# Kernel tuning notes

Measured on AMD Instinct MI355X. Metric: run time of the kernel, lower is better.

The kernel has to match this reference:

```python
import jax, jax.numpy as jnp
import numpy as np

B, N, D, H = 4, 1024, 256, 8  # batch, seq, in_dim(=per-head qkv_dim), n_heads


def setup_inputs() -> dict:
    key = jax.random.key(0)
    k1, k2, k3 = jax.random.split(key, 3)
    x = jax.random.normal(k1, (B, N, D), dtype=jnp.float32)
    Wqkv = jax.random.normal(k2, (D, 3 * D * H), dtype=jnp.float32) * 0.02
    bqkv = jnp.zeros((3 * D * H,), dtype=jnp.float32)
    W0 = jax.random.normal(k3, (D * H, D), dtype=jnp.float32) * 0.02
    b0 = jnp.zeros((D,), dtype=jnp.float32)
    return {"x": x, "Wqkv": Wqkv, "bqkv": bqkv, "W0": W0, "b0": b0}


def reference(x, Wqkv, bqkv, W0, b0):
    b, n, d = x.shape
    h = Wqkv.shape[1] // (3 * d)
    qkv = x @ Wqkv + bqkv                      # [b, n, 3*d*h]
    # Faithful to torch: raw row-major reinterpretation of the buffer.
    q, k, v = jnp.reshape(qkv, (3, b, n, d, h))
    score = jnp.einsum('bnqh,btqh->bnth', q, k) * (d ** -0.5)  # [b, n, n, h]
    attn = jax.nn.softmax(score, axis=1)       # softmax over query axis (dim=1), as in source
    # einsum 'bnnh,bnqh->bnqh' = diagonal of attn times v (faithful to source)
    av = jnp.einsum('bnnh,bnqh->bnqh', attn, v)  # [b, n, d, h]
    out = av.reshape(b, n, d * h) @ W0 + b0    # [b, n, d]
    return out
```

## Files before the change

kernel.cpp:

```cpp
#include <hip/hip_runtime.h>


#define SEGSZ 8388608

typedef short v8s __attribute__((ext_vector_type(8)));
typedef float v4f __attribute__((ext_vector_type(4)));

__device__ __forceinline__ ushort f2bf(float v) {
  union { float f; unsigned u; } x; x.f = v;
  const unsigned r = x.u + 0x7fff + ((x.u >> 16) & 1);
  return (ushort)(r >> 16);
}
__device__ __forceinline__ float bf2f(ushort v) {
  union { unsigned u; float f; } x; x.u = ((unsigned)v) << 16;
  return x.f;
}

#define GLOAD_LDS16(g, l)                                            \
  __builtin_amdgcn_global_load_lds(                                  \
      (const __attribute__((address_space(1))) void*)(g),            \
      (__attribute__((address_space(3))) void*)(l), 16, 0, 0)

__global__ __launch_bounds__(256) void prep(
    const float* __restrict__ X, const float* __restrict__ Wqkv,
    const float* __restrict__ W0, ushort* __restrict__ xb,
    ushort* __restrict__ whT, ushort* __restrict__ w0T) {
  __shared__ float T[64][65];
  const int tid = threadIdx.x;
  int bid = blockIdx.x;

  if (bid < 1024) {
    const size_t i = ((size_t)bid * 256 + tid) * 4;
    const float4 v = *(const float4*)&X[i];
    ushort4 hv = {f2bf(v.x), f2bf(v.y), f2bf(v.z), f2bf(v.w)};
    *(ushort4*)&xb[i] = hv;
    return;
  }
  bid -= 1024;
  if (bid < 384) {
    const int n0 = (bid % 96) * 64;
    const int k0 = (bid / 96) * 64;
    {
      const int row = tid >> 2;
      const int c0 = (tid & 3) * 16;
#pragma unroll
      for (int j = 0; j < 16; j += 4) {
        const float4 v = *(const float4*)&Wqkv[(size_t)(k0 + row) * 6144 + n0 + c0 + j];
        T[row][c0 + j + 0] = v.x; T[row][c0 + j + 1] = v.y;
        T[row][c0 + j + 2] = v.z; T[row][c0 + j + 3] = v.w;
      }
    }
    __syncthreads();
    {
      const int nn = tid >> 2;
      const int kk0 = (tid & 3) * 16;
      const int n = n0 + nn;
      const int seg = n >> 11, h = n & 7, d = (n & 2047) >> 3;
      const int p = seg * 2048 + h * 256 + d;
      ushort hv[16];
#pragma unroll
      for (int j = 0; j < 16; ++j) hv[j] = f2bf(T[kk0 + j][nn]);
      const size_t base = (size_t)p * 256 + k0 + kk0;
#pragma unroll
      for (int j = 0; j < 16; j += 8) *(v8s*)&whT[base + j] = *(v8s*)&hv[j];
    }
    return;
  }
  bid -= 384;
  {
    const int e0 = (bid & 3) * 64;
    const int k0 = (bid >> 2) * 64;
    {
      const int row = tid >> 2;
      const int c0 = (tid & 3) * 16;
#pragma unroll
      for (int j = 0; j < 16; j += 4) {
        const float4 v = *(const float4*)&W0[(size_t)(k0 + row) * 256 + e0 + c0 + j];
        T[row][c0 + j + 0] = v.x; T[row][c0 + j + 1] = v.y;
        T[row][c0 + j + 2] = v.z; T[row][c0 + j + 3] = v.w;
      }
    }
    __syncthreads();
    {
      const int ee = tid >> 2;
      const int kk0 = (tid & 3) * 16;
#pragma unroll
      for (int j = 0; j < 16; ++j) {
        const int k = k0 + kk0 + j;
        const int d = k >> 3, h = k & 7;
        w0T[(size_t)(e0 + ee) * 2048 + h * 256 + d] = f2bf(T[kk0 + j][ee]);
      }
    }
  }
}

__global__ __launch_bounds__(512) void qkv_mfma(
    const ushort* __restrict__ xb, const ushort* __restrict__ whT,
    const float* __restrict__ bias, ushort* __restrict__ qkvb) {
  __shared__ ushort As[256 * 32];
  __shared__ ushort Bh[128 * 32];
  const int tid = threadIdx.x;
  const int wave = tid >> 6, lane = tid & 63;
  const int quad = lane >> 4, l15 = lane & 15;
  const int c0 = blockIdx.x * 128;
  const int r0 = blockIdx.y * 256;
  const int wr = (wave >> 1) * 64;
  const int wc = (wave & 1) * 64;

  v4f acc[4][4] = {};

  for (int d0 = 0; d0 < 256; d0 += 32) {
#pragma unroll
    for (int h2 = 0; h2 < 2; ++h2) {
      const int rr = wave * 32 + h2 * 16;
      const int row = rr + (lane >> 2);
      GLOAD_LDS16(xb + (size_t)(r0 + row) * 256 + d0 + (lane & 3) * 8, &As[rr * 32]);
    }
    {
      const int rr = wave * 16;
      const int row = rr + (lane >> 2);
      GLOAD_LDS16(whT + (size_t)(c0 + row) * 256 + d0 + (lane & 3) * 8, &Bh[rr * 32]);
    }
    __syncthreads();

    v8s aF[4], bF[4];
#pragma unroll
    for (int i = 0; i < 4; ++i) {
      aF[i] = *(const v8s*)&As[(wr + i * 16 + l15) * 32 + quad * 8];
      bF[i] = *(const v8s*)&Bh[(wc + i * 16 + l15) * 32 + quad * 8];
    }
#pragma unroll
    for (int ri = 0; ri < 4; ++ri)
#pragma unroll
      for (int ci = 0; ci < 4; ++ci)
        acc[ri][ci] = __builtin_amdgcn_mfma_f32_16x16x32_bf16(
            aF[ri], bF[ci], acc[ri][ci], 0, 0, 0);
    __syncthreads();
  }

#pragma unroll
  for (int ci = 0; ci < 4; ++ci) {
    const int c = c0 + wc + ci * 16 + l15;
    const int cseg = c >> 11;
    const int h = (c & 2047) >> 8;
    const int d = c & 255;
    const float bv = bias[cseg * 2048 + d * 8 + h];
#pragma unroll
    for (int ri = 0; ri < 4; ++ri)
#pragma unroll
      for (int rg = 0; rg < 4; ++rg) {
        const int r = r0 + wr + ri * 16 + quad * 4 + rg;
        const int g = r * 3 + cseg;
        const int seg = g >> 12;
        const int tok = g & 4095;
        float val = acc[ri][ci][rg] + bv;
        if (seg == 0) val *= 0.0625f;
        qkvb[(size_t)seg * SEGSZ + (size_t)tok * 2048 + h * 256 + d] = f2bf(val);
      }
  }
}

__global__ __launch_bounds__(256) void scores_mfma(
    const ushort* __restrict__ qkvb, float* __restrict__ pl,
    float* __restrict__ sd_ws) {
  __shared__ ushort Ks[8 * 128 * 32];
  __shared__ ushort Qs[128 * 32];
  __shared__ float redL[2][2][64];

  const int tid = threadIdx.x;
  const int wave = tid >> 6, lane = tid & 63;
  const int quad = lane >> 4, l15 = lane & 15;
  const int bh = blockIdx.z * 8 + blockIdx.x;
  const int strip = blockIdx.y;
  const int tt0 = (strip >> 1) * 128;
  const int half = strip & 1;
  const int b = bh >> 3, h = bh & 7;
  const ushort* Qg = qkvb + (size_t)b * 1024 * 2048 + h * 256;
  const ushort* Kg = Qg + SEGSZ;

  const int wr = (wave >> 1) * 64;
  const int wc = (wave & 1) * 64;

#pragma unroll
  for (int c = 0; c < 8; ++c)
#pragma unroll
    for (int h2 = 0; h2 < 2; ++h2) {
      const int rr = wave * 32 + h2 * 16;
      const int row = rr + (lane >> 2);
      GLOAD_LDS16(Kg + (size_t)(tt0 + row) * 2048 + c * 32 + (lane & 3) * 8,
                  &Ks[c * 4096 + rr * 32]);
    }

  float colsum[4] = {0.f, 0.f, 0.f, 0.f};

  for (int i = 0; i < 4; ++i) {
    const int nn0 = half * 512 + i * 128;
    v4f acc[4][4] = {};
#pragma unroll
    for (int c = 0; c < 8; ++c) {
#pragma unroll
      for (int h2 = 0; h2 < 2; ++h2) {
        const int rr = wave * 32 + h2 * 16;
        const int row = rr + (lane >> 2);
        GLOAD_LDS16(Qg + (size_t)(nn0 + row) * 2048 + c * 32 + (lane & 3) * 8,
                    &Qs[rr * 32]);
      }
      __syncthreads();

      v8s aF[4], bF[4];
#pragma unroll
      for (int j = 0; j < 4; ++j) {
        aF[j] = *(const v8s*)&Qs[(wr + j * 16 + l15) * 32 + quad * 8];
        bF[j] = *(const v8s*)&Ks[c * 4096 + (wc + j * 16 + l15) * 32 + quad * 8];
      }
#pragma unroll
      for (int ri = 0; ri < 4; ++ri)
#pragma unroll
        for (int ci = 0; ci < 4; ++ci)
          acc[ri][ci] = __builtin_amdgcn_mfma_f32_16x16x32_bf16(
              aF[ri], bF[ci], acc[ri][ci], 0, 0, 0);
      __syncthreads();
    }
#pragma unroll
    for (int ci = 0; ci < 4; ++ci) {
      float s = 0.f;
#pragma unroll
      for (int ri = 0; ri < 4; ++ri)
#pragma unroll
        for (int rg = 0; rg < 4; ++rg) s += __expf(acc[ri][ci][rg]);
      colsum[ci] += s;
    }
    if (nn0 == tt0 && (wave == 0 || wave == 3) && quad == (l15 >> 2)) {
#pragma unroll
      for (int ri = 0; ri < 4; ++ri) {
        const int t = tt0 + (wave & 1) * 64 + ri * 16 + l15;
        sd_ws[(size_t)bh * 1024 + t] = acc[ri][ri][l15 & 3];
      }
    }
  }

#pragma unroll
  for (int ci = 0; ci < 4; ++ci) {
    colsum[ci] += __shfl_xor(colsum[ci], 16, 64);
    colsum[ci] += __shfl_xor(colsum[ci], 32, 64);
  }
  if (quad == 0) {
#pragma unroll
    for (int ci = 0; ci < 4; ++ci)
      redL[wave & 1][wave >> 1][ci * 16 + l15] = colsum[ci];
  }
  __syncthreads();
  if ((wave >> 1) == 0 && quad == 0) {
#pragma unroll
    for (int ci = 0; ci < 4; ++ci) {
      const int t = tt0 + (wave & 1) * 64 + ci * 16 + l15;
      const float l = colsum[ci] + redL[wave & 1][1][ci * 16 + l15];
      pl[((size_t)bh * 1024 + t) * 2 + half] = l;
    }
  }
}

template <bool ATOMIC>
__global__ __launch_bounds__(512) void av_mfma(
    const ushort* __restrict__ vb, const ushort* __restrict__ w0T,
    const float* __restrict__ pl, const float* __restrict__ sd,
    ushort* __restrict__ partial, float* __restrict__ out) {
  __shared__ ushort As[128 * 32];
  __shared__ ushort Bs[256 * 32];
  __shared__ float diagS[128];
  const int tid = threadIdx.x;
  const int wave = tid >> 6, lane = tid & 63;
  const int quad = lane >> 4, l15 = lane & 15;
  const int tok0 = blockIdx.x * 128;
  const int h = blockIdx.y;
  const int kbase = h * 256;
  const int wr = (wave >> 2) * 64;
  const int wc = (wave & 3) * 64;

  if (tid < 128) {
    const int bh = (tok0 >> 10) * 8 + h;
    const int t = (tok0 & 1023) + tid;
    const size_t base = ((size_t)bh * 1024 + t) * 2;
    diagS[tid] = __expf(sd[(size_t)bh * 1024 + t]) / (pl[base] + pl[base + 1]);
  }

  v4f acc[4][4] = {};

  for (int d0 = 0; d0 < 256; d0 += 32) {
    {
      const int rr = wave * 16;
      const int row = rr + (lane >> 2);
      GLOAD_LDS16(vb + (size_t)(tok0 + row) * 2048 + kbase + d0 + (lane & 3) * 8,
                  &As[rr * 32]);
    }
#pragma unroll
    for (int h2 = 0; h2 < 2; ++h2) {
      const int rr = wave * 32 + h2 * 16;
      const int row = rr + (lane >> 2);
      GLOAD_LDS16(w0T + (size_t)row * 2048 + kbase + d0 + (lane & 3) * 8,
                  &Bs[rr * 32]);
    }
    __syncthreads();

    v8s aF[4], bF[4];
#pragma unroll
    for (int i = 0; i < 4; ++i) {
      aF[i] = *(const v8s*)&As[(wr + i * 16 + l15) * 32 + quad * 8];
      bF[i] = *(const v8s*)&Bs[(wc + i * 16 + l15) * 32 + quad * 8];
    }
#pragma unroll
    for (int ri = 0; ri < 4; ++ri)
#pragma unroll
      for (int ci = 0; ci < 4; ++ci)
        acc[ri][ci] =
            __builtin_amdgcn_mfma_f32_16x16x32_bf16(aF[ri], bF[ci], acc[ri][ci], 0, 0, 0);
    __syncthreads();
  }

#pragma unroll
  for (int ri = 0; ri < 4; ++ri)
#pragma unroll
    for (int rg = 0; rg < 4; ++rg) {
      const int lrow = wr + ri * 16 + quad * 4 + rg;
      const int tok = tok0 + lrow;
      const float dg = diagS[lrow];
#pragma unroll
      for (int ci = 0; ci < 4; ++ci) {
        const int e = wc + ci * 16 + l15;
        const float val = acc[ri][ci][rg] * dg;
        if (ATOMIC)
          atomicAdd(&out[(size_t)tok * 256 + e], val);
        else
          partial[(size_t)h * 1048576 + (size_t)tok * 256 + e] = f2bf(val);
      }
    }
}

__global__ void init_out(const float* __restrict__ b0, float* __restrict__ out) {
  const int i = blockIdx.x * 256 + threadIdx.x;
  const int e0 = (i & 63) << 2;
  *(float4*)&out[(size_t)i * 4] = *(const float4*)&b0[e0];
}

__global__ void reduce_out(const ushort* __restrict__ partial,
                           const float* __restrict__ b0, float* __restrict__ out) {
  const int i = blockIdx.x * 256 + threadIdx.x;
  const int e0 = (i & 63) << 2;
  float4 a = *(const float4*)&b0[e0];
#pragma unroll
  for (int h = 0; h < 8; ++h) {
    const ushort4 p = *(const ushort4*)&partial[(size_t)h * 1048576 + (size_t)i * 4];
    a.x += bf2f(p.x); a.y += bf2f(p.y); a.z += bf2f(p.z); a.w += bf2f(p.w);
  }
  *(float4*)&out[(size_t)i * 4] = a;
}

extern "C" void kernel_launch(void* const* d_in, const int* in_sizes, int n_in,
                              void* d_out, int out_size, void* d_ws, size_t ws_size,
                              hipStream_t stream) {
  const float* x    = (const float*)d_in[0];
  const float* Wqkv = (const float*)d_in[1];
  const float* bqkv = (const float*)d_in[2];
  const float* W0   = (const float*)d_in[3];
  const float* b0   = (const float*)d_in[4];
  float* out = (float*)d_out;

  float*  pl   = (float*)d_ws;
  float*  sd   = pl + 65536;
  ushort* qkvb = (ushort*)(sd + 32768);
  ushort* xb   = qkvb + 3 * (size_t)SEGSZ;
  ushort* whT  = xb + 1048576;
  ushort* w0T  = whT + 1572864;
  ushort* partial = w0T + 524288;

  ushort* vb = qkvb + 2 * (size_t)SEGSZ;

  const size_t need_base =
      (size_t)(65536 + 32768) * 4 + (size_t)SEGSZ * 3 * 2 +
      (size_t)(1048576 + 1572864 + 524288) * 2;
  const bool full = ws_size >= need_base + (size_t)8 * 1048576 * 2;

  prep<<<1536, 256, 0, stream>>>(x, Wqkv, W0, xb, whT, w0T);
  qkv_mfma<<<dim3(48, 16), 512, 0, stream>>>(xb, whT, bqkv, qkvb);
  scores_mfma<<<dim3(8, 16, 4), 256, 0, stream>>>(qkvb, pl, sd);
  if (full) {
    av_mfma<false><<<dim3(32, 8), 512, 0, stream>>>(vb, w0T, pl, sd, partial, out);
    reduce_out<<<1024, 256, 0, stream>>>(partial, b0, out);
  } else {
    init_out<<<1024, 256, 0, stream>>>(b0, out);
    av_mfma<true><<<dim3(32, 8), 512, 0, stream>>>(vb, w0T, pl, sd, nullptr, out);
  }
}
```

Baseline: 142.4 us.

## Split score kernel into per-tile blocks with 32x32 MFMA and 8-way partial sums

The scores kernel now launches one block per 128x128 (query, key) tile, giving 4x more blocks. Each block streams both Q and K chunks instead of keeping a full K strip resident in LDS, which cuts LDS use from about 72KB to about 16KB and should raise occupancy. It also switches from 16x16x32 to 32x32x16 bf16 MFMA. Column exp-sums are written as 8 partials per token and summed in av_mfma, at the cost of reloading K per tile, more global traffic and a larger partial-sum buffer.

```diff
diff --git a/kernel.cpp b/kernel.cpp
--- a/kernel.cpp
+++ b/kernel.cpp
@@ -5,6 +5,7 @@
 
 typedef short v8s __attribute__((ext_vector_type(8)));
 typedef float v4f __attribute__((ext_vector_type(4)));
+typedef float v16f __attribute__((ext_vector_type(16)));
 
 __device__ __forceinline__ ushort f2bf(float v) {
   union { float f; unsigned u; } x; x.f = v;
@@ -163,17 +164,17 @@
 __global__ __launch_bounds__(256) void scores_mfma(
     const ushort* __restrict__ qkvb, float* __restrict__ pl,
     float* __restrict__ sd_ws) {
-  __shared__ ushort Ks[8 * 128 * 32];
   __shared__ ushort Qs[128 * 32];
+  __shared__ ushort Ks[128 * 32];
   __shared__ float redL[2][2][64];
 
   const int tid = threadIdx.x;
   const int wave = tid >> 6, lane = tid & 63;
-  const int quad = lane >> 4, l15 = lane & 15;
+  const int l31 = lane & 31, lh = lane >> 5;
   const int bh = blockIdx.z * 8 + blockIdx.x;
-  const int strip = blockIdx.y;
-  const int tt0 = (strip >> 1) * 128;
-  const int half = strip & 1;
+  const int tile = blockIdx.y;
+  const int tt0 = (tile >> 3) * 128;
+  const int nn0 = (tile & 7) * 128;
   const int b = bh >> 3, h = bh & 7;
   const ushort* Qg = qkvb + (size_t)b * 1024 * 2048 + h * 256;
   const ushort* Kg = Qg + SEGSZ;
@@ -181,81 +182,69 @@
   const int wr = (wave >> 1) * 64;
   const int wc = (wave & 1) * 64;
 
-#pragma unroll
-  for (int c = 0; c < 8; ++c)
+  v16f acc[2][2] = {};
+
+  for (int d0 = 0; d0 < 256; d0 += 32) {
 #pragma unroll
     for (int h2 = 0; h2 < 2; ++h2) {
       const int rr = wave * 32 + h2 * 16;
       const int row = rr + (lane >> 2);
-      GLOAD_LDS16(Kg + (size_t)(tt0 + row) * 2048 + c * 32 + (lane & 3) * 8,
-                  &Ks[c * 4096 + rr * 32]);
-    }
-
-  float colsum[4] = {0.f, 0.f, 0.f, 0.f};
-
-  for (int i = 0; i < 4; ++i) {
-    const int nn0 = half * 512 + i * 128;
-    v4f acc[4][4] = {};
-#pragma unroll
-    for (int c = 0; c < 8; ++c) {
-#pragma unroll
-      for (int h2 = 0; h2 < 2; ++h2) {
-        const int rr = wave * 32 + h2 * 16;
-        const int row = rr + (lane >> 2);
-        GLOAD_LDS16(Qg + (size_t)(nn0 + row) * 2048 + c * 32 + (lane & 3) * 8,
-                    &Qs[rr * 32]);
-      }
-      __syncthreads();
-
-      v8s aF[4], bF[4];
-#pragma unroll
-      for (int j = 0; j < 4; ++j) {
-        aF[j] = *(const v8s*)&Qs[(wr + j * 16 + l15) * 32 + quad * 8];
-        bF[j] = *(const v8s*)&Ks[c * 4096 + (wc + j * 16 + l15) * 32 + quad * 8];
-      }
-#pragma unroll
-      for (int ri = 0; ri < 4; ++ri)
-#pragma unroll
-        for (int ci = 0; ci < 4; ++ci)
-          acc[ri][ci] = __builtin_amdgcn_mfma_f32_16x16x32_bf16(
+      const int gcol = d0 + (lane & 3) * 8;
+      GLOAD_LDS16(Qg + (size_t)(nn0 + row) * 2048 + gcol, &Qs[rr * 32]);
+      GLOAD_LDS16(Kg + (size_t)(tt0 + row) * 2048 + gcol, &Ks[rr * 32]);
+    }
+    __syncthreads();
+
+#pragma unroll
+    for (int kk = 0; kk < 32; kk += 16) {
+      v8s aF[2], bF[2];
+#pragma unroll
+      for (int i = 0; i < 2; ++i) {
+        aF[i] = *(const v8s*)&Qs[(wr + i * 32 + l31) * 32 + kk + lh * 8];
+        bF[i] = *(const v8s*)&Ks[(wc + i * 32 + l31) * 32 + kk + lh * 8];
+      }
+#pragma unroll
+      for (int ri = 0; ri < 2; ++ri)
+#pragma unroll
+        for (int ci = 0; ci < 2; ++ci)
+          acc[ri][ci] = __builtin_amdgcn_mfma_f32_32x32x16_bf16(
               aF[ri], bF[ci], acc[ri][ci], 0, 0, 0);
-      __syncthreads();
-    }
-#pragma unroll
-    for (int ci = 0; ci < 4; ++ci) {
-      float s = 0.f;
-#pragma unroll
-      for (int ri = 0; ri < 4; ++ri)
-#pragma unroll
-        for (int rg = 0; rg < 4; ++rg) s += __expf(acc[ri][ci][rg]);
-      colsum[ci] += s;
-    }
-    if (nn0 == tt0 && (wave == 0 || wave == 3) && quad == (l15 >> 2)) {
-#pragma unroll
-      for (int ri = 0; ri < 4; ++ri) {
-        const int t = tt0 + (wave & 1) * 64 + ri * 16 + l15;
-        sd_ws[(size_t)bh * 1024 + t] = acc[ri][ri][l15 & 3];
-      }
-    }
-  }
-
-#pragma unroll
-  for (int ci = 0; ci < 4; ++ci) {
-    colsum[ci] += __shfl_xor(colsum[ci], 16, 64);
-    colsum[ci] += __shfl_xor(colsum[ci], 32, 64);
-  }
-  if (quad == 0) {
-#pragma unroll
-    for (int ci = 0; ci < 4; ++ci)
-      redL[wave & 1][wave >> 1][ci * 16 + l15] = colsum[ci];
+    }
+    __syncthreads();
+  }
+
+  float colsum[2];
+#pragma unroll
+  for (int ci = 0; ci < 2; ++ci) {
+    float s = 0.f;
+#pragma unroll
+    for (int ri = 0; ri < 2; ++ri)
+#pragma unroll
+      for (int rg = 0; rg < 16; ++rg) s += __expf(acc[ri][ci][rg]);
+    s += __shfl_xor(s, 32, 64);
+    colsum[ci] = s;
+  }
+  if (lh == 0) {
+#pragma unroll
+    for (int ci = 0; ci < 2; ++ci)
+      redL[wave & 1][wave >> 1][ci * 32 + l31] = colsum[ci];
   }
   __syncthreads();
-  if ((wave >> 1) == 0 && quad == 0) {
-#pragma unroll
-    for (int ci = 0; ci < 4; ++ci) {
-      const int t = tt0 + (wave & 1) * 64 + ci * 16 + l15;
-      const float l = colsum[ci] + redL[wave & 1][1][ci * 16 + l15];
-      pl[((size_t)bh * 1024 + t) * 2 + half] = l;
+  if ((wave >> 1) == 0 && lh == 0) {
+#pragma unroll
+    for (int ci = 0; ci < 2; ++ci) {
+      const int t = tt0 + (wave & 1) * 64 + ci * 32 + l31;
+      const float l = colsum[ci] + redL[wave & 1][1][ci * 32 + l31];
+      pl[((size_t)bh * 1024 + t) * 8 + (tile & 7)] = l;
+    }
+  }
+
+  if (tt0 == nn0 && (wave == 0 || wave == 3) && ((l31 >> 2) & 1) == lh) {
+    const int reg = (l31 & 3) + 4 * (l31 >> 3);
+#pragma unroll
+    for (int ri = 0; ri < 2; ++ri) {
+      const int t = tt0 + (wave & 1) * 64 + ri * 32 + l31;
+      sd_ws[(size_t)bh * 1024 + t] = acc[ri][ri][reg];
     }
   }
 }
@@ -280,8 +269,11 @@
   if (tid < 128) {
     const int bh = (tok0 >> 10) * 8 + h;
     const int t = (tok0 & 1023) + tid;
-    const size_t base = ((size_t)bh * 1024 + t) * 2;
-    diagS[tid] = __expf(sd[(size_t)bh * 1024 + t]) / (pl[base] + pl[base + 1]);
+    const size_t base = ((size_t)bh * 1024 + t) * 8;
+    float l = 0.f;
+#pragma unroll
+    for (int c = 0; c < 8; ++c) l += pl[base + c];
+    diagS[tid] = __expf(sd[(size_t)bh * 1024 + t]) / l;
   }
 
   v4f acc[4][4] = {};
@@ -366,7 +358,7 @@
   float* out = (float*)d_out;
 
   float*  pl   = (float*)d_ws;
-  float*  sd   = pl + 65536;
+  float*  sd   = pl + 262144;
   ushort* qkvb = (ushort*)(sd + 32768);
   ushort* xb   = qkvb + 3 * (size_t)SEGSZ;
   ushort* whT  = xb + 1048576;
@@ -376,13 +368,13 @@
   ushort* vb = qkvb + 2 * (size_t)SEGSZ;
 
   const size_t need_base =
-      (size_t)(65536 + 32768) * 4 + (size_t)SEGSZ * 3 * 2 +
+      (size_t)(262144 + 32768) * 4 + (size_t)SEGSZ * 3 * 2 +
       (size_t)(1048576 + 1572864 + 524288) * 2;
   const bool full = ws_size >= need_base + (size_t)8 * 1048576 * 2;
 
   prep<<<1536, 256, 0, stream>>>(x, Wqkv, W0, xb, whT, w0T);
   qkv_mfma<<<dim3(48, 16), 512, 0, stream>>>(xb, whT, bqkv, qkvb);
-  scores_mfma<<<dim3(8, 16, 4), 256, 0, stream>>>(qkvb, pl, sd);
+  scores_mfma<<<dim3(8, 64, 4), 256, 0, stream>>>(qkvb, pl, sd);
   if (full) {
     av_mfma<false><<<dim3(32, 8), 512, 0, stream>>>(vb, w0T, pl, sd, partial, out);
     reduce_out<<<1024, 256, 0, stream>>>(partial, b0, out);
```

Result: no change. 142.9 us (+0.3%).
